# Performance work log

Hardware: AMD Instinct MI355X
Metric: run time of the kernel (lower is better)

## Reference

```python
import jax, jax.numpy as jnp
import numpy as np
import math

B, S, D = 8, 4096, 768
H = 12
DH = D // H  # attention_head_size = 64


def setup_inputs() -> dict:
    key = jax.random.key(0)
    ks = jax.random.split(key, 6)
    sc = 0.02
    return {
        "hidden_states": jax.random.normal(ks[0], (B, S, D), dtype=jnp.float32),
        "attention_mask": jnp.zeros((B, 1, S), dtype=jnp.float32),
        "Wq": jax.random.normal(ks[1], (D, D), dtype=jnp.float32) * sc,
        "bq": jnp.zeros((D,), dtype=jnp.float32),
        "Wqa": jax.random.normal(ks[2], (H, D), dtype=jnp.float32) * sc,
        "bqa": jnp.zeros((H,), dtype=jnp.float32),
        "Wk": jax.random.normal(ks[3], (D, D), dtype=jnp.float32) * sc,
        "bk": jnp.zeros((D,), dtype=jnp.float32),
        "Wt": jax.random.normal(ks[4], (D, D), dtype=jnp.float32) * sc,
        "bt": jnp.zeros((D,), dtype=jnp.float32),
    }


def reference(hidden_states, attention_mask, Wq, bq, Wqa, bqa, Wk, bk, Wt, bt):
    inv_sqrt_dh = 1.0 / math.sqrt(DH)
    # projections (torch nn.Linear: x @ W.T + b)
    q = hidden_states @ Wq.T + bq            # [B,S,D]
    k = hidden_states @ Wk.T + bk            # [B,S,D]
    # query attention logits -> [B,H,S]
    qfs = jnp.swapaxes(q @ Wqa.T + bqa, 1, 2) * inv_sqrt_dh + attention_mask
    qw = jax.nn.softmax(qfs, axis=-1)        # [B,H,S]
    ql = jnp.swapaxes(q.reshape(B, S, H, DH), 1, 2)  # [B,H,S,DH]
    kl = jnp.swapaxes(k.reshape(B, S, H, DH), 1, 2)  # [B,H,S,DH]
    # global pooled query per head
    pooled_q = jnp.einsum('bhs,bhsd->bhd', qw, ql)   # [B,H,DH]
    # key attention over pooled query
    qks = jnp.einsum('bhsd,bhd->bhs', kl, pooled_q) * inv_sqrt_dh + attention_mask
    qkw = jax.nn.softmax(qks, axis=-1)       # [B,H,S]
    pooled_k = jnp.einsum('bhs,bhsd->bhd', qkw, kl)  # [B,H,DH]
    # gate query with pooled key, merge heads
    wv = pooled_k[:, :, None, :] * ql        # [B,H,S,DH]
    wv = jnp.swapaxes(wv, 1, 2).reshape(B, S, D)
    return wv @ Wt.T + bt + q
```

## Files before the change

### kernel.cpp

```cpp
#include <hip/hip_runtime.h>
#include <cstdint>
#include <cstddef>

#define S_LEN 4096
#define NB 8
#define NH 12
#define DMODEL 768
#define DHEAD 64
#define M_TOT (NB * S_LEN)
#define INV_SQRT_DH 0.125f
#define WSZ (DMODEL * DMODEL)

typedef __attribute__((ext_vector_type(4))) float f32x4;
typedef __attribute__((ext_vector_type(8))) short bf16x8;

__device__ inline float bf2f(unsigned short h) {
    union { unsigned int u; float f; } v; v.u = ((unsigned int)h) << 16; return v.f;
}
__device__ inline unsigned short f2bf(float f) {
    union { float f; unsigned int u; } v; v.f = f;
    unsigned int r = v.u + 0x7FFFu + ((v.u >> 16) & 1u);
    return (unsigned short)(r >> 16);
}

__device__ inline void gload_lds16(const unsigned short* gp, void* lp) {
    __builtin_amdgcn_global_load_lds((const __attribute__((address_space(1))) void*)gp,
                                     (__attribute__((address_space(3))) void*)lp,
                                     16, 0, 0);
}

__global__ void prep_all(const float* __restrict__ hs,
                         const float* __restrict__ Wq, const float* __restrict__ Wk,
                         const float* __restrict__ Wt, const float* __restrict__ Wqa,
                         const float* __restrict__ bq, const float* __restrict__ bk,
                         unsigned short* __restrict__ hs_bf,
                         unsigned short* __restrict__ Wqk_bf, unsigned short* __restrict__ Wt_bf,
                         unsigned short* __restrict__ Wqa_bf, float* __restrict__ bqk) {
    int bid = blockIdx.x;
    int t = threadIdx.x;
    if (bid < 24576) {
        int off = bid * 1024 + t * 4;
        float4 v = *(const float4*)(hs + off);
        ushort4 o;
        o.x = f2bf(v.x); o.y = f2bf(v.y); o.z = f2bf(v.z); o.w = f2bf(v.w);
        *(ushort4*)(hs_bf + off) = o;
        return;
    }
    bid -= 24576;
    if (bid < 1728) {
        const float* src = (bid < 576) ? Wq : ((bid < 1152) ? Wk : Wt);
        unsigned short* dst = (bid < 576) ? Wqk_bf : ((bid < 1152) ? (Wqk_bf + WSZ) : Wt_bf);
        int off = (bid % 576) * 1024 + t * 4;
        float4 v = *(const float4*)(src + off);
        ushort4 o;
        o.x = f2bf(v.x); o.y = f2bf(v.y); o.z = f2bf(v.z); o.w = f2bf(v.w);
        *(ushort4*)(dst + off) = o;
    } else if (bid < 1740) {
        int off = (bid - 1728) * 1024 + t * 4;
        int h = off / DMODEL;
        ushort4 o = {0, 0, 0, 0};
        if (h < NH) {
            float4 v = *(const float4*)(Wqa + off);
            o.x = f2bf(v.x); o.y = f2bf(v.y); o.z = f2bf(v.z); o.w = f2bf(v.w);
        }
        *(ushort4*)(Wqa_bf + off) = o;
    } else {
        int off = (bid - 1740) * 1024 + t * 4;
        if (off < 2 * DMODEL) {
            const float* src = (off < DMODEL) ? (bq + off) : (bk + off - DMODEL);
            *(float4*)(bqk + off) = *(const float4*)src;
        }
    }
}

#define PH_MID() do { __builtin_amdgcn_s_barrier(); \
    asm volatile("s_waitcnt lgkmcnt(0)"); \
    __builtin_amdgcn_sched_barrier(0); \
    __builtin_amdgcn_s_setprio(1); } while (0)
#define PH_END() do { __builtin_amdgcn_s_setprio(0); \
    __builtin_amdgcn_s_barrier(); } while (0)

#define STG_A(q, kt, BO) gload_lds16(pA + (size_t)((q) * 64) * 768 + (kt) * 64, \
                                     lds + (BO) + (q) * 8192 + wOff)
#define STG_B(q, kt, BO) gload_lds16(pB + (size_t)((q) * 64) * 768 + (kt) * 64, \
                                     lds + (BO) + 32768 + (q) * 8192 + wOff)

#define LD_A(mh, BO) do { _Pragma("unroll") for (int mm = 0; mm < 4; ++mm) { \
    a[mm][0] = *(const bf16x8*)(lds + (BO) + aRd0 + ((mh) * 4 + mm) * 2048); \
    a[mm][1] = *(const bf16x8*)(lds + (BO) + aRd1 + ((mh) * 4 + mm) * 2048); } } while (0)
#define LD_B(nh, BO) do { _Pragma("unroll") for (int nn = 0; nn < 2; ++nn) { \
    b[(nh) * 2 + nn][0] = *(const bf16x8*)(lds + (BO) + bRd0 + ((nh) * 2 + nn) * 2048); \
    b[(nh) * 2 + nn][1] = *(const bf16x8*)(lds + (BO) + bRd1 + ((nh) * 2 + nn) * 2048); } } while (0)
#define MFMAQ(mh, nh) do { _Pragma("unroll") for (int mm = 0; mm < 4; ++mm) \
    _Pragma("unroll") for (int nn = 0; nn < 2; ++nn) { \
        acc[(mh) * 4 + mm][(nh) * 2 + nn] = __builtin_amdgcn_mfma_f32_16x16x32_bf16( \
            a[mm][0], b[(nh) * 2 + nn][0], acc[(mh) * 4 + mm][(nh) * 2 + nn], 0, 0, 0); \
        acc[(mh) * 4 + mm][(nh) * 2 + nn] = __builtin_amdgcn_mfma_f32_16x16x32_bf16( \
            a[mm][1], b[(nh) * 2 + nn][1], acc[(mh) * 4 + mm][(nh) * 2 + nn], 0, 0, 0); } } while (0)

__global__ __launch_bounds__(512, 2) void gemm8(
    const unsigned short* __restrict__ A,
    const unsigned short* __restrict__ Bw,
    const float* __restrict__ bias,
    unsigned short* __restrict__ outBf, int ldoBf,
    int ntn)
{
    __shared__ __align__(16) char lds[131072];

    int nwg = gridDim.x;
    int bid = blockIdx.x;
    int cpx = nwg >> 3;
    int swz = (bid & 7) * cpx + (bid >> 3);
    int bidn = swz % ntn, bidm = swz / ntn;
    int m0 = bidm * 256, n0 = bidn * 256;

    int t = threadIdx.x;
    int w = t >> 6, lane = t & 63;
    int lr = lane & 15, lk = lane >> 4;
    int wr = w >> 2, wc = w & 3;
    int wOff = w << 10;

    int srow = t >> 3;
    int sblk = (t & 7) ^ (srow & 7);
    const unsigned short* pA = A + (size_t)(m0 + srow) * 768 + sblk * 8;
    const unsigned short* pB = Bw + (size_t)(n0 + srow) * 768 + sblk * 8;

    int sx = lr & 7;
    int aRd0 = (wr * 128 + lr) * 128 + ((0 + lk) ^ sx) * 16;
    int aRd1 = (wr * 128 + lr) * 128 + ((4 + lk) ^ sx) * 16;
    int bRd0 = 32768 + (wc * 64 + lr) * 128 + ((0 + lk) ^ sx) * 16;
    int bRd1 = 32768 + (wc * 64 + lr) * 128 + ((4 + lk) ^ sx) * 16;

    f32x4 acc[8][4];
#pragma unroll
    for (int m = 0; m < 8; ++m)
#pragma unroll
        for (int n = 0; n < 4; ++n)
            acc[m][n] = (f32x4){0.f, 0.f, 0.f, 0.f};
    bf16x8 a[4][2], b[4][2];

    STG_A(0, 0, 0); STG_A(1, 0, 0); STG_A(2, 0, 0); STG_A(3, 0, 0);
    STG_B(0, 0, 0); STG_B(1, 0, 0); STG_B(2, 0, 0); STG_B(3, 0, 0);
    STG_A(0, 1, 65536); STG_A(2, 1, 65536);
    STG_B(0, 1, 65536); STG_B(1, 1, 65536); STG_B(2, 1, 65536); STG_B(3, 1, 65536);
    asm volatile("s_waitcnt vmcnt(6)");
    __builtin_amdgcn_s_barrier();

    for (int i = 0; i < 6; ++i) {
        int ktE = 2 * i, ktO = 2 * i + 1;
        int s2 = (i < 5);
        LD_A(0, 0); LD_B(0, 0);
        STG_A(1, ktO, 65536); STG_A(3, ktO, 65536);
        PH_MID(); MFMAQ(0, 0); PH_END();
        LD_B(1, 0);
        if (s2) { STG_A(0, ktE + 2, 0); STG_A(2, ktE + 2, 0); }
        PH_MID(); MFMAQ(0, 1); PH_END();
        LD_A(1, 0);
        if (s2) { STG_B(0, ktE + 2, 0); STG_B(1, ktE + 2, 0); }
        PH_MID(); MFMAQ(1, 1); PH_END();
        if (s2) { STG_B(2, ktE + 2, 0); STG_B(3, ktE + 2, 0); }
        PH_MID(); MFMAQ(1, 0);
        __builtin_amdgcn_s_setprio(0);
        if (s2) { asm volatile("s_waitcnt vmcnt(6)"); }
        else    { asm volatile("s_waitcnt vmcnt(0)"); }
        __builtin_amdgcn_s_barrier();
        LD_A(0, 65536); LD_B(0, 65536);
        if (s2) { STG_A(1, ktE + 2, 0); STG_A(3, ktE + 2, 0); }
        PH_MID(); MFMAQ(0, 0); PH_END();
        LD_B(1, 65536);
        if (s2) { STG_A(0, ktO + 2, 65536); STG_A(2, ktO + 2, 65536); }
        PH_MID(); MFMAQ(0, 1); PH_END();
        LD_A(1, 65536);
        if (s2) { STG_B(0, ktO + 2, 65536); STG_B(1, ktO + 2, 65536); }
        PH_MID(); MFMAQ(1, 1); PH_END();
        if (s2) { STG_B(2, ktO + 2, 65536); STG_B(3, ktO + 2, 65536); }
        PH_MID(); MFMAQ(1, 0);
        __builtin_amdgcn_s_setprio(0);
        if (s2) { asm volatile("s_waitcnt vmcnt(6)"); }
        __builtin_amdgcn_s_barrier();
    }

#pragma unroll
    for (int m = 0; m < 8; ++m) {
        int gr0 = m0 + wr * 128 + m * 16 + lk * 4;
#pragma unroll
        for (int n = 0; n < 4; ++n) {
            int gc = n0 + wc * 64 + n * 16 + lr;
            float bv = bias[gc];
#pragma unroll
            for (int r = 0; r < 4; ++r) {
                int gr = gr0 + r;
                outBf[(size_t)gr * ldoBf + gc] = f2bf(acc[m][n][r] + bv);
            }
        }
    }
}

#define STG5_A(q, kt, SB) gload_lds16(pA + (size_t)((q) * 32) * 1536 + (kt) * 64, \
                                      lds + (SB) + (q) * 4096 + tOff)
#define STG5_B(q, kt, SB) gload_lds16(pB + (size_t)((q) * 32) * 768 + (kt) * 64, \
                                      lds + (SB) + 16384 + (q) * 4096 + tOff)
#define LD5(ARD, BRD, BUF) do { _Pragma("unroll") for (int mm = 0; mm < 4; ++mm) \
        a[mm] = *(const bf16x8*)(lds + (BUF) + (ARD) + mm * 2048); \
    _Pragma("unroll") for (int nn = 0; nn < 2; ++nn) \
        b[nn] = *(const bf16x8*)(lds + (BUF) + (BRD) + nn * 2048); } while (0)
#define MFMA5() do { _Pragma("unroll") for (int mm = 0; mm < 4; ++mm) \
    _Pragma("unroll") for (int nn = 0; nn < 2; ++nn) \
        acc[mm][nn] = __builtin_amdgcn_mfma_f32_16x16x32_bf16( \
            a[mm], b[nn], acc[mm][nn], 0, 0, 0); } while (0)

#define TILE5(t, BUF, SB) do { \
     \
    LD5(aRd0, bRd0, BUF); \
    if ((t) <= 9) { STG5_A(0, (t) + 2, SB); STG5_A(1, (t) + 2, SB); \
                    STG5_A(2, (t) + 2, SB); STG5_A(3, (t) + 2, SB); } \
    PH_MID(); MFMA5(); PH_END(); \
     \
    LD5(aRd1, bRd1, BUF); \
    if ((t) <= 9) { STG5_B(0, (t) + 2, SB); STG5_B(1, (t) + 2, SB); } \
    PH_MID(); MFMA5(); \
    __builtin_amdgcn_s_setprio(0); \
    if ((t) <= 9)       { asm volatile("s_waitcnt vmcnt(6)"); } \
    else if ((t) == 10) { asm volatile("s_waitcnt vmcnt(0)"); } \
    __builtin_amdgcn_s_barrier(); \
} while (0)

__global__ __launch_bounds__(256, 2) void gemm2k(
    const unsigned short* __restrict__ A,
    const unsigned short* __restrict__ W8,
    const float* __restrict__ bias,
    float* __restrict__ outF,
    const unsigned short* __restrict__ resid)
{
    __shared__ __align__(16) char lds[73728];

    int nwg = gridDim.x;
    int bid = blockIdx.x;
    int cpx = nwg >> 3;
    int swz = (bid & 7) * cpx + (bid >> 3);
    int bidn = swz % 12, bidm = swz / 12;
    int m0 = bidm * 128, n0 = bidn * 64;

    const unsigned short* Bw = W8 + (size_t)(m0 >> 12) * WSZ;

    int t = threadIdx.x;
    int w = t >> 6, lane = t & 63;
    int lr = lane & 15, lk = lane >> 4;
    int wr = w >> 1, wc = w & 1;
    int tOff = w << 10;

    int srow = t >> 3;
    int sblk = (t & 7) ^ (srow & 7);
    const unsigned short* pA = A + (size_t)(m0 + srow) * 1536 + sblk * 8;
    const unsigned short* pB = Bw + (size_t)(n0 + srow) * 768 + sblk * 8;

    int sx = lr & 7;
    int aRd0 = (wr * 64 + lr) * 128 + ((0 + lk) ^ sx) * 16;
    int aRd1 = (wr * 64 + lr) * 128 + ((4 + lk) ^ sx) * 16;
    int bRd0 = 16384 + (wc * 32 + lr) * 128 + ((0 + lk) ^ sx) * 16;
    int bRd1 = 16384 + (wc * 32 + lr) * 128 + ((4 + lk) ^ sx) * 16;

    f32x4 acc[4][2];
#pragma unroll
    for (int m = 0; m < 4; ++m)
#pragma unroll
        for (int n = 0; n < 2; ++n)
            acc[m][n] = (f32x4){0.f, 0.f, 0.f, 0.f};
    bf16x8 a[4], b[2];

    STG5_A(0, 0, 0); STG5_A(1, 0, 0); STG5_A(2, 0, 0); STG5_A(3, 0, 0);
    STG5_B(0, 0, 0); STG5_B(1, 0, 0);
    STG5_A(0, 1, 24576); STG5_A(1, 1, 24576); STG5_A(2, 1, 24576); STG5_A(3, 1, 24576);
    STG5_B(0, 1, 24576); STG5_B(1, 1, 24576);
    asm volatile("s_waitcnt vmcnt(6)");
    __builtin_amdgcn_s_barrier();

    for (int ii = 0; ii < 4; ++ii) {
        int tb = ii * 3;
        TILE5(tb + 0, 0,     49152);
        TILE5(tb + 1, 24576, 0);
        TILE5(tb + 2, 49152, 24576);
    }

#pragma unroll
    for (int m = 0; m < 4; ++m) {
        int gr0 = m0 + wr * 64 + m * 16 + lk * 4;
#pragma unroll
        for (int n = 0; n < 2; ++n) {
            int gc = n0 + wc * 32 + n * 16 + lr;
            float bv = bias[gc];
#pragma unroll
            for (int r = 0; r < 4; ++r) {
                int gr = gr0 + r;
                float v = acc[m][n][r] + bv + bf2f(resid[(size_t)gr * 1536 + gc]);
                outF[(size_t)gr * DMODEL + gc] = v;
            }
        }
    }
}

__global__ __launch_bounds__(256) void qfs_kernel(
    const unsigned short* __restrict__ q, int ldq,
    const unsigned short* __restrict__ wqa,
    const float* __restrict__ bqa,
    const float* __restrict__ mask,
    float* __restrict__ qfs)
{
    int t = threadIdx.x;
    int w = t >> 6, lane = t & 63;
    int lr = lane & 15, lk = lane >> 4;
    int m0 = blockIdx.x * 64 + w * 16;

    f32x4 acc = (f32x4){0.f, 0.f, 0.f, 0.f};
    for (int k0 = 0; k0 < DMODEL; k0 += 32) {
        bf16x8 av = *(const bf16x8*)&q[(size_t)(m0 + lr) * ldq + k0 + lk * 8];
        bf16x8 bv = *(const bf16x8*)&wqa[lr * DMODEL + k0 + lk * 8];
        acc = __builtin_amdgcn_mfma_f32_16x16x32_bf16(av, bv, acc, 0, 0, 0);
    }
    if (lr < NH) {
        float bv = bqa[lr];
#pragma unroll
        for (int r = 0; r < 4; ++r) {
            int m = m0 + lk * 4 + r;
            int b_ = m >> 12;
            int s = m & (S_LEN - 1);
            qfs[((size_t)b_ * NH + lr) * S_LEN + s] = acc[r] * INV_SQRT_DH + bv + mask[b_ * S_LEN + s];
        }
    }
}

__global__ __launch_bounds__(256) void pool1_kernel(
    const float* __restrict__ logits,
    const unsigned short* __restrict__ qk,
    float* __restrict__ parts)
{
    int bid = blockIdx.x;
    int bh = bid >> 3, c = bid & 7;
    int b = bh / NH, h = bh % NH;
    int s0 = c * 512;
    int t = threadIdx.x;

    __shared__ float w[512];
    __shared__ float red[8];
    __shared__ float part[4][64];

    const float* lg = logits + (size_t)bh * S_LEN + s0;
    float l0 = lg[t], l1 = lg[t + 256];
    float m = fmaxf(l0, l1);
#pragma unroll
    for (int off = 32; off; off >>= 1) m = fmaxf(m, __shfl_xor(m, off));
    if ((t & 63) == 0) red[t >> 6] = m;
    __syncthreads();
    float M = fmaxf(fmaxf(red[0], red[1]), fmaxf(red[2], red[3]));
    float w0 = __expf(l0 - M), w1 = __expf(l1 - M);
    w[t] = w0; w[t + 256] = w1;
    float z = w0 + w1;
#pragma unroll
    for (int off = 32; off; off >>= 1) z += __shfl_xor(z, off);
    if ((t & 63) == 0) red[4 + (t >> 6)] = z;
    __syncthreads();
    float Z = red[4] + red[5] + red[6] + red[7];

    int dblk = t & 7, rgrp = t >> 3;
    const unsigned short* xp = qk + ((size_t)(b * S_LEN + s0)) * 1536 + h * DHEAD + dblk * 8;
    float acc[8];
#pragma unroll
    for (int e = 0; e < 8; ++e) acc[e] = 0.f;
    for (int j = 0; j < 16; ++j) {
        int r = j * 32 + rgrp;
        bf16x8 v = *(const bf16x8*)(xp + (size_t)r * 1536);
        float wr = w[r];
#pragma unroll
        for (int e = 0; e < 8; ++e) acc[e] += wr * bf2f((unsigned short)v[e]);
    }
#pragma unroll
    for (int off = 8; off <= 32; off <<= 1)
#pragma unroll
        for (int e = 0; e < 8; ++e) acc[e] += __shfl_xor(acc[e], off);
    if ((t & 63) < 8) {
#pragma unroll
        for (int e = 0; e < 8; ++e) part[t >> 6][(t & 7) * 8 + e] = acc[e];
    }
    __syncthreads();
    float* dst = parts + ((size_t)bh * 8 + c) * 72;
    if (t < 64) dst[t] = part[0][t] + part[1][t] + part[2][t] + part[3][t];
    else if (t == 64) dst[64] = M;
    else if (t == 65) dst[65] = Z;
}

__global__ __launch_bounds__(256) void pool2_kernel(
    const float* __restrict__ parts1,
    const unsigned short* __restrict__ qk,
    const float* __restrict__ mask,
    float* __restrict__ parts2)
{
    int bid = blockIdx.x;
    int bh = bid >> 3, c = bid & 7;
    int b = bh / NH, h = bh % NH;
    int s0 = c * 512;
    int t = threadIdx.x;

    __shared__ float pq[64];
    __shared__ float w[512];
    __shared__ float red[8];
    __shared__ float part[4][64];

    if (t < 64) {
        const float* p1 = parts1 + (size_t)bh * 8 * 72;
        float M1 = -1e30f;
#pragma unroll
        for (int cc = 0; cc < 8; ++cc) M1 = fmaxf(M1, p1[cc * 72 + 64]);
        float Z1 = 0.f, a1 = 0.f;
#pragma unroll
        for (int cc = 0; cc < 8; ++cc) {
            float f = __expf(p1[cc * 72 + 64] - M1);
            Z1 += f * p1[cc * 72 + 65];
            a1 += f * p1[cc * 72 + t];
        }
        pq[t] = a1 / Z1;
    }
    __syncthreads();

    int dblk = t & 7, rgrp = t >> 3;
    float pq8[8];
#pragma unroll
    for (int e = 0; e < 8; ++e) pq8[e] = pq[dblk * 8 + e];

    const unsigned short* kp = qk + ((size_t)(b * S_LEN + s0)) * 1536 + DMODEL + h * DHEAD + dblk * 8;

    for (int j = 0; j < 16; ++j) {
        int r = j * 32 + rgrp;
        bf16x8 v = *(const bf16x8*)(kp + (size_t)r * 1536);
        float d = 0.f;
#pragma unroll
        for (int e = 0; e < 8; ++e) d += bf2f((unsigned short)v[e]) * pq8[e];
        d += __shfl_xor(d, 1); d += __shfl_xor(d, 2); d += __shfl_xor(d, 4);
        if (dblk == 0) w[r] = d * INV_SQRT_DH + mask[b * S_LEN + s0 + r];
    }
    __syncthreads();

    float l0 = w[t], l1 = w[t + 256];
    float m = fmaxf(l0, l1);
#pragma unroll
    for (int off = 32; off; off >>= 1) m = fmaxf(m, __shfl_xor(m, off));
    if ((t & 63) == 0) red[t >> 6] = m;
    __syncthreads();
    float M = fmaxf(fmaxf(red[0], red[1]), fmaxf(red[2], red[3]));
    float w0 = __expf(l0 - M), w1 = __expf(l1 - M);
    float z = w0 + w1;
#pragma unroll
    for (int off = 32; off; off >>= 1) z += __shfl_xor(z, off);
    if ((t & 63) == 0) red[4 + (t >> 6)] = z;
    __syncthreads();
    w[t] = w0; w[t + 256] = w1;
    __syncthreads();
    float Z = red[4] + red[5] + red[6] + red[7];

    float acc[8];
#pragma unroll
    for (int e = 0; e < 8; ++e) acc[e] = 0.f;
    for (int j = 0; j < 16; ++j) {
        int r = j * 32 + rgrp;
        bf16x8 v = *(const bf16x8*)(kp + (size_t)r * 1536);
        float wr = w[r];
#pragma unroll
        for (int e = 0; e < 8; ++e) acc[e] += wr * bf2f((unsigned short)v[e]);
    }
#pragma unroll
    for (int off = 8; off <= 32; off <<= 1)
#pragma unroll
        for (int e = 0; e < 8; ++e) acc[e] += __shfl_xor(acc[e], off);
    if ((t & 63) < 8) {
#pragma unroll
        for (int e = 0; e < 8; ++e) part[t >> 6][(t & 7) * 8 + e] = acc[e];
    }
    __syncthreads();
    float* dst = parts2 + ((size_t)bh * 8 + c) * 72;
    if (t < 64) dst[t] = part[0][t] + part[1][t] + part[2][t] + part[3][t];
    else if (t == 64) dst[64] = M;
    else if (t == 65) dst[65] = Z;
}

__global__ __launch_bounds__(256) void gatedw_kernel(
    const float* __restrict__ parts2,
    const unsigned short* __restrict__ Wt_bf,
    unsigned short* __restrict__ W8)
{
    int bid = blockIdx.x;
    int b = bid / 96, rg = bid % 96;
    int t = threadIdx.x;

    __shared__ float mhc[96], Mh[12], fac[96], zh[12], pk[768];

    if (t < 96) mhc[t] = parts2[((size_t)(b * NH + t / 8) * 8 + (t & 7)) * 72 + 64];
    __syncthreads();
    if (t < 12) {
        float M = -1e30f;
#pragma unroll
        for (int cc = 0; cc < 8; ++cc) M = fmaxf(M, mhc[t * 8 + cc]);
        Mh[t] = M;
    }
    __syncthreads();
    if (t < 96) fac[t] = __expf(mhc[t] - Mh[t / 8]);
    __syncthreads();
    if (t < 12) {
        float Zm = 0.f;
#pragma unroll
        for (int cc = 0; cc < 8; ++cc)
            Zm += fac[t * 8 + cc] * parts2[((size_t)(b * NH + t) * 8 + cc) * 72 + 65];
        zh[t] = Zm;
    }
    __syncthreads();
#pragma unroll
    for (int j = 0; j < 3; ++j) {
        int col = t + 256 * j;
        int h = col >> 6, d = col & 63;
        const float* p2 = parts2 + (size_t)(b * NH + h) * 8 * 72;
        float v = 0.f;
#pragma unroll
        for (int cc = 0; cc < 8; ++cc) v += fac[h * 8 + cc] * p2[cc * 72 + d];
        pk[col] = v / zh[h];
    }
    __syncthreads();
#pragma unroll
    for (int j = 0; j < 3; ++j) {
        int idx = j * 2048 + t * 8;
        int r = rg * 8 + idx / DMODEL, k = idx % DMODEL;
        bf16x8 wv = *(const bf16x8*)(Wt_bf + (size_t)r * DMODEL + k);
        bf16x8 o;
#pragma unroll
        for (int e = 0; e < 8; ++e)
            o[e] = (short)f2bf(bf2f((unsigned short)wv[e]) * pk[k + e]);
        *(bf16x8*)(W8 + (size_t)b * WSZ + (size_t)r * DMODEL + k) = o;
    }
}

extern "C" void kernel_launch(void* const* d_in, const int* in_sizes, int n_in,
                              void* d_out, int out_size, void* d_ws, size_t ws_size,
                              hipStream_t stream) {
    const float* hs   = (const float*)d_in[0];
    const float* mask = (const float*)d_in[1];
    const float* Wq   = (const float*)d_in[2];
    const float* bq   = (const float*)d_in[3];
    const float* Wqa  = (const float*)d_in[4];
    const float* bqa  = (const float*)d_in[5];
    const float* Wk   = (const float*)d_in[6];
    const float* bk   = (const float*)d_in[7];
    const float* Wt   = (const float*)d_in[8];
    const float* bt   = (const float*)d_in[9];
    float* out = (float*)d_out;

    char* ws = (char*)d_ws;
    unsigned short* qk_bf  = (unsigned short*)(ws);
    unsigned short* hs_bf  = (unsigned short*)(ws + 100663296);
    unsigned short* W8     = hs_bf;
    unsigned short* Wqk_bf = (unsigned short*)(ws + 150994944);
    unsigned short* Wt_bf  = (unsigned short*)(ws + 153354240);
    unsigned short* Wqa_bf = (unsigned short*)(ws + 154533888);
    float* bqk    = (float*)(ws + 154558464);
    float* qfs    = (float*)(ws + 154564608);
    float* parts1 = (float*)(ws + 156137472);
    float* parts2 = (float*)(ws + 156358656);

    prep_all<<<26318, 256, 0, stream>>>(hs, Wq, Wk, Wt, Wqa, bq, bk,
                                        hs_bf, Wqk_bf, Wt_bf, Wqa_bf, bqk);

    gemm8<<<(M_TOT / 256) * 6, 512, 0, stream>>>(
        hs_bf, Wqk_bf, bqk, qk_bf, 2 * DMODEL, 6);

    qfs_kernel<<<M_TOT / 64, 256, 0, stream>>>(qk_bf, 2 * DMODEL, Wqa_bf, bqa, mask, qfs);
    pool1_kernel<<<NB * NH * 8, 256, 0, stream>>>(qfs, qk_bf, parts1);
    pool2_kernel<<<NB * NH * 8, 256, 0, stream>>>(parts1, qk_bf, mask, parts2);
    gatedw_kernel<<<NB * 96, 256, 0, stream>>>(parts2, Wt_bf, W8);

    gemm2k<<<(M_TOT / 128) * 12, 256, 0, stream>>>(
        qk_bf, W8, bt, out, qk_bf);
}
```

Baseline: 213.4 us.

## Enlarge output GEMM tile to 256x128 with 512 threads and single-phase k-loop

Replaces the final projection GEMM's 128x64 tile (256 threads) with a 256x128 tile (512 threads, 8 waves), each wave computing 64x64. Larger tiles raise arithmetic intensity and cut redundant global and LDS staging of A and W. The two half-k phases per tile are merged: all fragments are loaded first, then 32 MFMAs run back to back. LDS use doubles to 144KB, which likely allows only one block per CU despite the launch bound of 2, and register pressure rises.

```diff
diff --git a/kernel.cpp b/kernel.cpp
--- a/kernel.cpp
+++ b/kernel.cpp
@@ -196,50 +196,26 @@
     }
 }
 
-#define STG5_A(q, kt, SB) gload_lds16(pA + (size_t)((q) * 32) * 1536 + (kt) * 64, \
-                                      lds + (SB) + (q) * 4096 + tOff)
-#define STG5_B(q, kt, SB) gload_lds16(pB + (size_t)((q) * 32) * 768 + (kt) * 64, \
-                                      lds + (SB) + 16384 + (q) * 4096 + tOff)
-#define LD5(ARD, BRD, BUF) do { _Pragma("unroll") for (int mm = 0; mm < 4; ++mm) \
-        a[mm] = *(const bf16x8*)(lds + (BUF) + (ARD) + mm * 2048); \
-    _Pragma("unroll") for (int nn = 0; nn < 2; ++nn) \
-        b[nn] = *(const bf16x8*)(lds + (BUF) + (BRD) + nn * 2048); } while (0)
-#define MFMA5() do { _Pragma("unroll") for (int mm = 0; mm < 4; ++mm) \
-    _Pragma("unroll") for (int nn = 0; nn < 2; ++nn) \
-        acc[mm][nn] = __builtin_amdgcn_mfma_f32_16x16x32_bf16( \
-            a[mm], b[nn], acc[mm][nn], 0, 0, 0); } while (0)
-
-#define TILE5(t, BUF, SB) do { \
-     \
-    LD5(aRd0, bRd0, BUF); \
-    if ((t) <= 9) { STG5_A(0, (t) + 2, SB); STG5_A(1, (t) + 2, SB); \
-                    STG5_A(2, (t) + 2, SB); STG5_A(3, (t) + 2, SB); } \
-    PH_MID(); MFMA5(); PH_END(); \
-     \
-    LD5(aRd1, bRd1, BUF); \
-    if ((t) <= 9) { STG5_B(0, (t) + 2, SB); STG5_B(1, (t) + 2, SB); } \
-    PH_MID(); MFMA5(); \
-    __builtin_amdgcn_s_setprio(0); \
-    if ((t) <= 9)       { asm volatile("s_waitcnt vmcnt(6)"); } \
-    else if ((t) == 10) { asm volatile("s_waitcnt vmcnt(0)"); } \
-    __builtin_amdgcn_s_barrier(); \
-} while (0)
-
-__global__ __launch_bounds__(256, 2) void gemm2k(
+#define STG6_A(q, kt, SB) gload_lds16(pA + (size_t)((q) * 64) * 1536 + (kt) * 64, \
+                                      lds + (SB) + (q) * 8192 + wOff)
+#define STG6_B(q, kt, SB) gload_lds16(pB + (size_t)((q) * 64) * 768 + (kt) * 64, \
+                                      lds + (SB) + 32768 + (q) * 8192 + wOff)
+
+__global__ __launch_bounds__(512, 2) void gemm3(
     const unsigned short* __restrict__ A,
     const unsigned short* __restrict__ W8,
     const float* __restrict__ bias,
     float* __restrict__ outF,
     const unsigned short* __restrict__ resid)
 {
-    __shared__ __align__(16) char lds[73728];
+    __shared__ __align__(16) char lds[147456];
 
     int nwg = gridDim.x;
     int bid = blockIdx.x;
     int cpx = nwg >> 3;
     int swz = (bid & 7) * cpx + (bid >> 3);
-    int bidn = swz % 12, bidm = swz / 12;
-    int m0 = bidm * 128, n0 = bidn * 64;
+    int bidn = swz % 6, bidm = swz / 6;
+    int m0 = bidm * 256, n0 = bidn * 128;
 
     const unsigned short* Bw = W8 + (size_t)(m0 >> 12) * WSZ;
 
@@ -247,7 +223,7 @@
     int w = t >> 6, lane = t & 63;
     int lr = lane & 15, lk = lane >> 4;
     int wr = w >> 1, wc = w & 1;
-    int tOff = w << 10;
+    int wOff = w << 10;
 
     int srow = t >> 3;
     int sblk = (t & 7) ^ (srow & 7);
@@ -257,37 +233,58 @@
     int sx = lr & 7;
     int aRd0 = (wr * 64 + lr) * 128 + ((0 + lk) ^ sx) * 16;
     int aRd1 = (wr * 64 + lr) * 128 + ((4 + lk) ^ sx) * 16;
-    int bRd0 = 16384 + (wc * 32 + lr) * 128 + ((0 + lk) ^ sx) * 16;
-    int bRd1 = 16384 + (wc * 32 + lr) * 128 + ((4 + lk) ^ sx) * 16;
-
-    f32x4 acc[4][2];
+    int bRd0 = 32768 + (wc * 64 + lr) * 128 + ((0 + lk) ^ sx) * 16;
+    int bRd1 = 32768 + (wc * 64 + lr) * 128 + ((4 + lk) ^ sx) * 16;
+
+    f32x4 acc[4][4];
 #pragma unroll
     for (int m = 0; m < 4; ++m)
 #pragma unroll
-        for (int n = 0; n < 2; ++n)
+        for (int n = 0; n < 4; ++n)
             acc[m][n] = (f32x4){0.f, 0.f, 0.f, 0.f};
-    bf16x8 a[4], b[2];
-
-    STG5_A(0, 0, 0); STG5_A(1, 0, 0); STG5_A(2, 0, 0); STG5_A(3, 0, 0);
-    STG5_B(0, 0, 0); STG5_B(1, 0, 0);
-    STG5_A(0, 1, 24576); STG5_A(1, 1, 24576); STG5_A(2, 1, 24576); STG5_A(3, 1, 24576);
-    STG5_B(0, 1, 24576); STG5_B(1, 1, 24576);
+    bf16x8 a[4][2], b[4][2];
+
+    STG6_A(0, 0, 0); STG6_A(1, 0, 0); STG6_A(2, 0, 0); STG6_A(3, 0, 0);
+    STG6_B(0, 0, 0); STG6_B(1, 0, 0);
+    STG6_A(0, 1, 49152); STG6_A(1, 1, 49152); STG6_A(2, 1, 49152); STG6_A(3, 1, 49152);
+    STG6_B(0, 1, 49152); STG6_B(1, 1, 49152);
     asm volatile("s_waitcnt vmcnt(6)");
     __builtin_amdgcn_s_barrier();
 
+#define TILE6(tt, BUF, SB) do { \
+    if ((tt) <= 9) { STG6_A(0, (tt) + 2, SB); STG6_A(1, (tt) + 2, SB); \
+                     STG6_A(2, (tt) + 2, SB); STG6_A(3, (tt) + 2, SB); \
+                     STG6_B(0, (tt) + 2, SB); STG6_B(1, (tt) + 2, SB); } \
+    _Pragma("unroll") for (int mm = 0; mm < 4; ++mm) { \
+        a[mm][0] = *(const bf16x8*)(lds + (BUF) + aRd0 + mm * 2048); \
+        a[mm][1] = *(const bf16x8*)(lds + (BUF) + aRd1 + mm * 2048); } \
+    _Pragma("unroll") for (int nn = 0; nn < 4; ++nn) { \
+        b[nn][0] = *(const bf16x8*)(lds + (BUF) + bRd0 + nn * 2048); \
+        b[nn][1] = *(const bf16x8*)(lds + (BUF) + bRd1 + nn * 2048); } \
+    PH_MID(); \
+    _Pragma("unroll") for (int mm = 0; mm < 4; ++mm) \
+    _Pragma("unroll") for (int nn = 0; nn < 4; ++nn) { \
+        acc[mm][nn] = __builtin_amdgcn_mfma_f32_16x16x32_bf16(a[mm][0], b[nn][0], acc[mm][nn], 0, 0, 0); \
+        acc[mm][nn] = __builtin_amdgcn_mfma_f32_16x16x32_bf16(a[mm][1], b[nn][1], acc[mm][nn], 0, 0, 0); } \
+    __builtin_amdgcn_s_setprio(0); \
+    if ((tt) <= 9)       { asm volatile("s_waitcnt vmcnt(6)"); } \
+    else if ((tt) == 10) { asm volatile("s_waitcnt vmcnt(0)"); } \
+    __builtin_amdgcn_s_barrier(); \
+} while (0)
+
     for (int ii = 0; ii < 4; ++ii) {
         int tb = ii * 3;
-        TILE5(tb + 0, 0,     49152);
-        TILE5(tb + 1, 24576, 0);
-        TILE5(tb + 2, 49152, 24576);
+        TILE6(tb + 0, 0,     98304);
+        TILE6(tb + 1, 49152, 0);
+        TILE6(tb + 2, 98304, 49152);
     }
 
 #pragma unroll
     for (int m = 0; m < 4; ++m) {
         int gr0 = m0 + wr * 64 + m * 16 + lk * 4;
 #pragma unroll
-        for (int n = 0; n < 2; ++n) {
-            int gc = n0 + wc * 32 + n * 16 + lr;
+        for (int n = 0; n < 4; ++n) {
+            int gc = n0 + wc * 64 + n * 16 + lr;
             float bv = bias[gc];
 #pragma unroll
             for (int r = 0; r < 4; ++r) {
@@ -573,6 +570,6 @@
     pool2_kernel<<<NB * NH * 8, 256, 0, stream>>>(parts1, qk_bf, mask, parts2);
     gatedw_kernel<<<NB * 96, 256, 0, stream>>>(parts2, Wt_bf, W8);
 
-    gemm2k<<<(M_TOT / 128) * 12, 256, 0, stream>>>(
+    gemm3<<<(M_TOT / 256) * 6, 512, 0, stream>>>(
         qk_bf, W8, bt, out, qk_bf);
 }
```

After: 213.5 us. Within noise of the previous version (+0.1%).
